# Optimization experiments

Hardware: AMD Instinct MI355X
Metric: run time of the kernel (lower is better)

The kernel has to match this reference:

```python
import jax, jax.numpy as jnp
import numpy as np
from jax import lax

N = 32768      # total nodes (8 graphs x 4096)
E = 262144     # edges (avg degree 8)
B = 8          # graphs in batch
TW = 25        # time window
H = 128        # hidden features
L = 6          # GNN layers
NV = 1         # n_variables (pos_t only)
SD = 1         # spatial dim
TMAX, TMIN, RES_T = 4.0, 0.0, 250.0
BD_LOW, BD_UP = 0.0, 16.0
EPS = 1e-5


def swish(x):
    return x * jax.nn.sigmoid(x)


def setup_inputs() -> dict:
    key = jax.random.key(0)
    ks = jax.random.split(key, 32)
    s = 0.05
    u = jax.random.normal(ks[0], (N, TW), jnp.float32)
    pos_t = jax.random.uniform(ks[1], (N, 1), jnp.float32) * TMAX
    pos_x = jax.random.uniform(ks[2], (N, 1), jnp.float32) * BD_UP
    pos = jnp.concatenate([pos_t, pos_x], axis=-1)
    edge_index = jax.random.randint(ks[3], (2, E), 0, N, jnp.int64)
    batch = jnp.repeat(jnp.arange(B, dtype=jnp.int64), N // B)
    d_in = TW + SD + NV          # 27
    d_msg = 2 * H + TW + SD + NV  # 282
    d_upd = H + H + NV            # 257
    We1 = jax.random.normal(ks[4], (d_in, H), jnp.float32) * s
    be1 = jnp.zeros((H,), jnp.float32)
    We2 = jax.random.normal(ks[5], (H, H), jnp.float32) * s
    be2 = jnp.zeros((H,), jnp.float32)
    Wm1 = jax.random.normal(ks[6], (L, d_msg, H), jnp.float32) * s
    bm1 = jnp.zeros((L, H), jnp.float32)
    Wm2 = jax.random.normal(ks[7], (L, H, H), jnp.float32) * s
    bm2 = jnp.zeros((L, H), jnp.float32)
    Wu1 = jax.random.normal(ks[8], (L, d_upd, H), jnp.float32) * s
    bu1 = jnp.zeros((L, H), jnp.float32)
    Wu2 = jax.random.normal(ks[9], (L, H, H), jnp.float32) * s
    bu2 = jnp.zeros((L, H), jnp.float32)
    Wc1 = jax.random.normal(ks[10], (8, 1, 16), jnp.float32) * s  # OIH
    bc1 = jnp.zeros((8,), jnp.float32)
    Wc2 = jax.random.normal(ks[11], (1, 8, 14), jnp.float32) * s
    bc2 = jnp.zeros((1,), jnp.float32)
    return dict(u=u, pos=pos, edge_index=edge_index, batch=batch,
                We1=We1, be1=be1, We2=We2, be2=be2,
                Wm1=Wm1, bm1=bm1, Wm2=Wm2, bm2=bm2,
                Wu1=Wu1, bu1=bu1, Wu2=Wu2, bu2=bu2,
                Wc1=Wc1, bc1=bc1, Wc2=Wc2, bc2=bc2)


def _mpnn(u, pos, edge_index, batch, We1, be1, We2, be2,
          Wm1, bm1, Wm2, bm2, Wu1, bu1, Wu2, bu2, Wc1, bc1, Wc2, bc2):
    src = edge_index[0]   # j (source)
    tgt = edge_index[1]   # i (target)
    pos_t = pos[:, 0:1] / TMAX
    pos_x = (pos[:, 1:] - BD_LOW) / (BD_UP - BD_LOW)
    variables = pos_t  # eq_variables empty -> only normalized time

    node_input = jnp.concatenate([u, pos_x, variables], axis=-1)  # [N, 27]
    h = swish(node_input @ We1 + be1)
    h = swish(h @ We2 + be2)

    # in-degree for scatter-mean (empty targets -> 0 like PyG mean)
    cnt = jnp.zeros((N,), jnp.float32).at[tgt].add(1.0)
    cnt = jnp.maximum(cnt, 1.0)[:, None]
    # per-graph node counts for InstanceNorm
    gcnt = jax.ops.segment_sum(jnp.ones((N,), jnp.float32), batch, num_segments=B)[:, None]

    u_diff_e = u[tgt] - u[src]          # [E, TW]
    p_diff_e = pos_x[tgt] - pos_x[src]  # [E, SD]
    var_i_e = variables[tgt]            # [E, NV]

    for l in range(L):
        # message: gather -> MLP per edge
        m_in = jnp.concatenate([h[tgt], h[src], u_diff_e, p_diff_e, var_i_e], axis=-1)  # [E, 282]
        msg = swish(m_in @ Wm1[l] + bm1[l])
        msg = swish(msg @ Wm2[l] + bm2[l])
        # scatter-mean aggregate onto targets
        agg = jax.ops.segment_sum(msg, tgt, num_segments=N) / cnt  # [N, H]
        # node update MLP, residual (in_features == out_features)
        up = jnp.concatenate([h, agg, variables], axis=-1)  # [N, 257]
        up = swish(up @ Wu1[l] + bu1[l])
        up = swish(up @ Wu2[l] + bu2[l])
        h = h + up
        # InstanceNorm per graph (no affine), biased variance
        mean = jax.ops.segment_sum(h, batch, num_segments=B) / gcnt      # [B, H]
        sq = jax.ops.segment_sum(h * h, batch, num_segments=B) / gcnt    # [B, H]
        var = sq - mean * mean
        h = (h - mean[batch]) / jnp.sqrt(var[batch] + EPS)

    # output CNN: tw=25 branch
    hc = h[:, None, :]  # [N, 1, 128]
    dn = ('NCH', 'OIH', 'NCH')
    c = lax.conv_general_dilated(hc, Wc1, (3,), 'VALID', dimension_numbers=dn) + bc1[None, :, None]
    c = swish(c)
    c = lax.conv_general_dilated(c, Wc2, (1,), 'VALID', dimension_numbers=dn) + bc2[None, :, None]
    diff = c[:, 0, :]  # [N, 25]

    dt = (TMAX - TMIN) / RES_T
    dt_cum = jnp.arange(1, TW + 1, dtype=jnp.float32) * dt  # cumsum of ones*dt
    out = u[:, -1:] + dt_cum[None, :] * diff
    return out


def reference(u, pos, edge_index, batch, We1, be1, We2, be2,
              Wm1, bm1, Wm2, bm2, Wu1, bu1, Wu2, bu2, Wc1, bc1, Wc2, bc2):
    return _mpnn(u, pos, edge_index, batch, We1, be1, We2, be2,
                 Wm1, bm1, Wm2, bm2, Wu1, bu1, Wu2, bu2, Wc1, bc1, Wc2, bc2)
```

## Files before the change

kernel.cpp:

```cpp
#include <hip/hip_runtime.h>
#include <stdint.h>

#define N_NODES 32768
#define N_EDGES 262144
#define NB 8
#define TW 25

typedef __attribute__((ext_vector_type(8))) short short8;
typedef __attribute__((ext_vector_type(4))) float floatx4;

#if defined(__has_builtin)
#if __has_builtin(__builtin_amdgcn_cvt_pk_bf16_f32)
#define HAVE_CVT_PK_BF16 1
#endif
#endif

__device__ __forceinline__ float swishf(float x) {
    return x * __builtin_amdgcn_rcpf(1.0f + __expf(-x));
}

__device__ __forceinline__ unsigned short f2bf(float x) {
    union { float f; unsigned u; } v; v.f = x;
    unsigned r = v.u + 0x7FFFu + ((v.u >> 16) & 1u);
    return (unsigned short)(r >> 16);
}
__device__ __forceinline__ unsigned pkbf(float a, float b) {
#ifdef HAVE_CVT_PK_BF16
    typedef __attribute__((ext_vector_type(2))) __bf16 bf16x2;
    union { bf16x2 v; unsigned u; } cv;
    cv.v = __builtin_amdgcn_cvt_pk_bf16_f32(a, b);
    return cv.u;
#else
    return (unsigned)f2bf(a) | ((unsigned)f2bf(b) << 16);
#endif
}
__device__ __forceinline__ float bf2f(unsigned short b) {
    union { unsigned u; float f; } v; v.u = ((unsigned)b) << 16; return v.f;
}
__device__ __forceinline__ float bflo(unsigned w) {
    union { unsigned u; float f; } v; v.u = w << 16; return v.f;
}
__device__ __forceinline__ float bfhi(unsigned w) {
    union { unsigned u; float f; } v; v.u = w & 0xffff0000u; return v.f;
}

__global__ void init_kernel(const float* __restrict__ pos, const float* __restrict__ u,
                            float* __restrict__ posx, float* __restrict__ post,
                            unsigned short* __restrict__ feat) {
    int i = blockIdx.x * 256 + threadIdx.x;
    if (i < N_NODES) {
        float pt = pos[i * 2 + 0] * 0.25f;
        float px = pos[i * 2 + 1] * 0.0625f;
        post[i] = pt;
        posx[i] = px;
        unsigned short f[32];
        #pragma unroll
        for (int k = 0; k < 25; ++k) f[k] = f2bf(u[(size_t)i * 25 + k]);
        f[25] = f2bf(px);
        f[26] = f2bf(pt);
        #pragma unroll
        for (int k = 27; k < 32; ++k) f[k] = 0;
        #pragma unroll
        for (int j = 0; j < 4; ++j)
            *(uint4*)(feat + (size_t)i * 32 + j * 8) = *(uint4*)&f[j * 8];
    }
}

__global__ void deg_kernel(const int* __restrict__ tgt, int* __restrict__ deg) {
    int i = blockIdx.x * 256 + threadIdx.x;
    if (i < N_EDGES) atomicAdd(&deg[tgt[i]], 1);
}

__global__ __launch_bounds__(1024) void scan_kernel(const int* __restrict__ deg,
                                                    int* __restrict__ cursor) {
    __shared__ int ps[1024];
    int t = threadIdx.x;
    int base = t * 32;
    int tot = 0;
    for (int i = 0; i < 32; ++i) tot += deg[base + i];
    ps[t] = tot;
    __syncthreads();
    for (int off = 1; off < 1024; off <<= 1) {
        int v = (t >= off) ? ps[t - off] : 0;
        __syncthreads();
        ps[t] += v;
        __syncthreads();
    }
    int run = ps[t] - tot;
    for (int i = 0; i < 32; ++i) {
        cursor[base + i] = run;
        run += deg[base + i];
    }
}

__global__ void scatter_kernel(const int* __restrict__ src, const int* __restrict__ tgt,
                               int* __restrict__ cursor,
                               int* __restrict__ src_s, int* __restrict__ tgt_s) {
    int i = blockIdx.x * 256 + threadIdx.x;
    if (i < N_EDGES) {
        int tg = tgt[i];
        int p = atomicAdd(&cursor[tg], 1);
        src_s[p] = src[i];
        tgt_s[p] = tg;
    }
}

__global__ __launch_bounds__(256) void pack_kernel(const float* __restrict__ W,
                                                   unsigned short* __restrict__ Wp,
                                                   int Kreal, int Kc, int total) {
    int id = blockIdx.x * 256 + threadIdx.x;
    if (id >= total) return;
    int lane = id & 63;
    int t8 = (id >> 6) & 7;
    int rest = id >> 9;
    int c = rest % Kc;
    int l = rest / Kc;
    int n = t8 * 16 + (lane & 15);
    int kb = c * 32 + (lane >> 4) * 8;
    short8 v;
    #pragma unroll
    for (int j = 0; j < 8; ++j) {
        int k = kb + j;
        float x = (k < Kreal) ? W[((size_t)l * Kreal + k) * 128 + n] : 0.f;
        v[j] = (short)f2bf(x);
    }
    *(short8*)(Wp + (size_t)id * 8) = v;
}

__global__ __launch_bounds__(256) void pack_cat_kernel(const float* __restrict__ Wm1,
                                                       unsigned short* __restrict__ Wp) {
    int id = blockIdx.x * 256 + threadIdx.x;
    if (id >= 30720) return;
    int lane = id & 63;
    int tile = (id >> 6) & 15;
    int rest = id >> 10;
    int c = rest % 5;
    int l = rest / 5;
    int n = tile * 16 + (lane & 15);
    int col = n & 127;
    bool isT = n < 128;
    int kb = c * 32 + (lane >> 4) * 8;
    const float* W = Wm1 + (size_t)l * 283 * 128;
    short8 v;
    #pragma unroll
    for (int j = 0; j < 8; ++j) {
        int k = kb + j;
        float x = 0.f;
        if (k < 128) {
            x = W[(size_t)(isT ? k : 128 + k) * 128 + col];
        } else if (k < 155) {
            int row = 256 + (k - 128);
            x = W[(size_t)row * 128 + col];
            if (!isT) x = (row == 282) ? 0.f : -x;
        }
        v[j] = (short)f2bf(x);
    }
    *(short8*)(Wp + (size_t)id * 8) = v;
}

__global__ __launch_bounds__(256) void encoder_kernel(
    const float* __restrict__ u, const float* __restrict__ posx,
    const float* __restrict__ post,
    const float* __restrict__ We1, const float* __restrict__ be1,
    const float* __restrict__ We2, const float* __restrict__ be2,
    unsigned short* __restrict__ hraw, float* __restrict__ agg)
{
    __shared__ __align__(16) float As_[64 * 36];
    __shared__ __align__(16) float Ws[32 * 128];
    __shared__ __align__(16) float Ms[64 * 128];

    int t = threadIdx.x;
    int n0 = blockIdx.x * 64;
    int rg = t >> 5, cg = t & 31;

    {
        int r = t & 63, cseg = t >> 6;
        float4 z = make_float4(0.f, 0.f, 0.f, 0.f);
        #pragma unroll
        for (int j = 0; j < 8; ++j)
            *(float4*)(agg + (size_t)(n0 + r) * 128 + cseg * 32 + j * 4) = z;
    }

    float acc[8][4] = {};
    {
        int kk = t >> 3, cb = (t & 7) * 16;
        #pragma unroll
        for (int j = 0; j < 4; ++j) {
            float4 w = make_float4(0.f, 0.f, 0.f, 0.f);
            if (kk < 27) w = *(const float4*)&We1[kk * 128 + cb + j * 4];
            *(float4*)&Ws[kk * 128 + cb + j * 4] = w;
        }
        int el = t >> 2, kb = (t & 3) * 8, n = n0 + el;
        float v[8];
        #pragma unroll
        for (int j = 0; j < 8; ++j) {
            int k = kb + j;
            float x = 0.f;
            if (k < 25) x = u[n * 25 + k];
            else if (k == 25) x = posx[n];
            else if (k == 26) x = post[n];
            v[j] = x;
        }
        #pragma unroll
        for (int j = 0; j < 8; j += 4)
            *(float4*)&As_[el * 36 + kb + j] = make_float4(v[j], v[j+1], v[j+2], v[j+3]);
        __syncthreads();
        #pragma unroll 4
        for (int kk2 = 0; kk2 < 32; ++kk2) {
            float4 b = *(const float4*)&Ws[kk2 * 128 + cg * 4];
            float a[8];
            #pragma unroll
            for (int i = 0; i < 8; ++i) a[i] = As_[(rg * 8 + i) * 36 + kk2];
            #pragma unroll
            for (int i = 0; i < 8; ++i) {
                acc[i][0] += a[i] * b.x; acc[i][1] += a[i] * b.y;
                acc[i][2] += a[i] * b.z; acc[i][3] += a[i] * b.w;
            }
        }
        __syncthreads();
    }
    {
        float4 b1 = *(const float4*)&be1[cg * 4];
        #pragma unroll
        for (int i = 0; i < 8; ++i) {
            float4 m;
            m.x = swishf(acc[i][0] + b1.x);
            m.y = swishf(acc[i][1] + b1.y);
            m.z = swishf(acc[i][2] + b1.z);
            m.w = swishf(acc[i][3] + b1.w);
            *(float4*)&Ms[(rg * 8 + i) * 128 + cg * 4] = m;
        }
        __syncthreads();
    }
    float acc2[8][4] = {};
    for (int k0 = 0; k0 < 128; k0 += 32) {
        int kk = t >> 3, cb = (t & 7) * 16;
        #pragma unroll
        for (int j = 0; j < 4; ++j)
            *(float4*)&Ws[kk * 128 + cb + j * 4] =
                *(const float4*)&We2[(k0 + kk) * 128 + cb + j * 4];
        __syncthreads();
        #pragma unroll 4
        for (int kk2 = 0; kk2 < 32; ++kk2) {
            float4 b = *(const float4*)&Ws[kk2 * 128 + cg * 4];
            float a[8];
            #pragma unroll
            for (int i = 0; i < 8; ++i) a[i] = Ms[(rg * 8 + i) * 128 + (k0 + kk2)];
            #pragma unroll
            for (int i = 0; i < 8; ++i) {
                acc2[i][0] += a[i] * b.x; acc2[i][1] += a[i] * b.y;
                acc2[i][2] += a[i] * b.z; acc2[i][3] += a[i] * b.w;
            }
        }
        __syncthreads();
    }
    {
        float4 b2 = *(const float4*)&be2[cg * 4];
        #pragma unroll
        for (int i = 0; i < 8; ++i) {
            int n = n0 + rg * 8 + i;
            float4 o;
            o.x = swishf(acc2[i][0] + b2.x);
            o.y = swishf(acc2[i][1] + b2.y);
            o.z = swishf(acc2[i][2] + b2.z);
            o.w = swishf(acc2[i][3] + b2.w);
            uint2 pk;
            pk.x = pkbf(o.x, o.y);
            pk.y = pkbf(o.z, o.w);
            *(uint2*)(hraw + (size_t)n * 128 + cg * 4) = pk;
        }
    }
}

__global__ __launch_bounds__(512, 4) void premsg_kernel(
    const unsigned short* __restrict__ hraw,
    const float* __restrict__ stats, int donorm,
    const unsigned short* __restrict__ feat,
    const unsigned short* __restrict__ Wp, const float* __restrict__ b1,
    unsigned short* __restrict__ h_bf,
    unsigned short* __restrict__ At, unsigned short* __restrict__ As)
{
    __shared__ __align__(16) unsigned short A[64 * 168];
    __shared__ float mean_s[128];
    __shared__ float rstd_s[128];

    int t = threadIdx.x;
    int n0 = blockIdx.x * 64;
    int bidx = n0 >> 12;

    if (t < 128) {
        float mn = 0.f, rs = 1.f;
        if (donorm) {
            float s1 = stats[bidx * 128 + t] * (1.f / 4096.f);
            float s2 = stats[(NB + bidx) * 128 + t] * (1.f / 4096.f);
            mn = s1;
            rs = rsqrtf(s2 - s1 * s1 + 1e-5f);
        }
        mean_s[t] = mn;
        rstd_s[t] = rs;
    }
    __syncthreads();

    {
        int r = t & 63, cseg = t >> 6;
        int n = n0 + r;
        uint4 raw0 = *(const uint4*)(hraw + (size_t)n * 128 + cseg * 16);
        uint4 raw1 = *(const uint4*)(hraw + (size_t)n * 128 + cseg * 16 + 8);
        unsigned pk[8];
        #pragma unroll
        for (int j = 0; j < 8; ++j) {
            unsigned word = (j < 4) ? ((const unsigned*)&raw0)[j]
                                    : ((const unsigned*)&raw1)[j - 4];
            int c0 = cseg * 16 + j * 2;
            float v0 = (bf2f((unsigned short)(word & 0xffffu)) - mean_s[c0]) * rstd_s[c0];
            float v1 = (bf2f((unsigned short)(word >> 16)) - mean_s[c0 + 1]) * rstd_s[c0 + 1];
            pk[j] = pkbf(v0, v1);
        }
        *(uint4*)(A + r * 168 + cseg * 16)     = *(uint4*)&pk[0];
        *(uint4*)(A + r * 168 + cseg * 16 + 8) = *(uint4*)&pk[4];
        *(uint4*)(h_bf + (size_t)n * 128 + cseg * 16)     = *(uint4*)&pk[0];
        *(uint4*)(h_bf + (size_t)n * 128 + cseg * 16 + 8) = *(uint4*)&pk[4];
        if (cseg < 2) {
            uint4 f0 = *(const uint4*)(feat + (size_t)n * 32 + cseg * 16);
            uint4 f1 = *(const uint4*)(feat + (size_t)n * 32 + cseg * 16 + 8);
            *(uint4*)(A + r * 168 + 128 + cseg * 16)     = f0;
            *(uint4*)(A + r * 168 + 128 + cseg * 16 + 8) = f1;
        }
    }
    __syncthreads();

    int w = t >> 6, lane = t & 63, q = lane >> 4, m = lane & 15;
    floatx4 accT[4] = {};
    floatx4 accS[4] = {};
    #pragma unroll
    for (int c = 0; c < 5; ++c) {
        short8 bT = *(const short8*)(Wp + ((size_t)(c * 16 + w) * 64 + lane) * 8);
        short8 bS = *(const short8*)(Wp + ((size_t)(c * 16 + 8 + w) * 64 + lane) * 8);
        #pragma unroll
        for (int g2 = 0; g2 < 4; ++g2) {
            short8 a = *(const short8*)(A + (g2 * 16 + m) * 168 + c * 32 + q * 8);
            accT[g2] = __builtin_amdgcn_mfma_f32_16x16x32_bf16(a, bT, accT[g2], 0, 0, 0);
            accS[g2] = __builtin_amdgcn_mfma_f32_16x16x32_bf16(a, bS, accS[g2], 0, 0, 0);
        }
    }
    int col = w * 16 + m;
    float bv = b1[col];
    #pragma unroll
    for (int g2 = 0; g2 < 4; ++g2) {
        #pragma unroll
        for (int r = 0; r < 4; ++r) {
            int row = g2 * 16 + q * 4 + r;
            At[(size_t)(n0 + row) * 128 + col] = f2bf(accT[g2][r] + bv);
            As[(size_t)(n0 + row) * 128 + col] = f2bf(accS[g2][r]);
        }
    }
}

__global__ __launch_bounds__(256, 8) void message_kernel(
    const unsigned short* __restrict__ At, const unsigned short* __restrict__ As,
    const int* __restrict__ src_s, const int* __restrict__ tgt_s,
    const unsigned short* __restrict__ W2p, const float* __restrict__ b2,
    float* __restrict__ agg, float* __restrict__ stats)
{
    __shared__ __align__(16) unsigned short Cs[64 * 132];
    __shared__ int tgtS[64];

    int t = threadIdx.x;
    int e0 = blockIdx.x * 64;
    if (blockIdx.x == 0) {
        float4 z = make_float4(0.f, 0.f, 0.f, 0.f);
        *(float4*)&stats[t * 8] = z;
        *(float4*)&stats[t * 8 + 4] = z;
    }
    if (t < 64) tgtS[t] = tgt_s[e0 + t];
    __syncthreads();

    int w = t >> 6, lane = t & 63, q = lane >> 4, m = lane & 15;
    int erow = w * 16 + m;
    int e = e0 + erow;
    int gg = tgtS[erow];
    int ss = src_s[e];

    const unsigned short* atp = At + (size_t)gg * 128 + q * 8;
    const unsigned short* asp = As + (size_t)ss * 128 + q * 8;
    uint4 wa[4], wb[4];
    #pragma unroll
    for (int c = 0; c < 4; ++c) {
        wa[c] = *(const uint4*)(atp + c * 32);
        wb[c] = *(const uint4*)(asp + c * 32);
    }
    short8 af[4];
    #pragma unroll
    for (int c = 0; c < 4; ++c) {
        const unsigned* ua = (const unsigned*)&wa[c];
        const unsigned* ub = (const unsigned*)&wb[c];
        union { unsigned u[4]; short8 s; } pk_;
        #pragma unroll
        for (int j = 0; j < 4; ++j) {
            float lo = swishf(bflo(ua[j]) + bflo(ub[j]));
            float hi = swishf(bfhi(ua[j]) + bfhi(ub[j]));
            pk_.u[j] = pkbf(lo, hi);
        }
        af[c] = pk_.s;
    }

    floatx4 acc[8] = {};
    #pragma unroll
    for (int c = 0; c < 4; ++c) {
        #pragma unroll
        for (int t8 = 0; t8 < 8; ++t8) {
            short8 b = *(const short8*)(W2p + ((size_t)(c * 8 + t8) * 64 + lane) * 8);
            acc[t8] = __builtin_amdgcn_mfma_f32_16x16x32_bf16(af[c], b, acc[t8], 0, 0, 0);
        }
    }

    #pragma unroll
    for (int t8 = 0; t8 < 8; ++t8) {
        float bv = b2[t8 * 16 + m];
        unsigned p01 = pkbf(swishf(acc[t8][0] + bv), swishf(acc[t8][1] + bv));
        unsigned p23 = pkbf(swishf(acc[t8][2] + bv), swishf(acc[t8][3] + bv));
        int rb = (w * 16 + q * 4) * 132 + t8 * 16 + m;
        Cs[rb]           = (unsigned short)p01;
        Cs[rb + 132]     = (unsigned short)(p01 >> 16);
        Cs[rb + 2 * 132] = (unsigned short)p23;
        Cs[rb + 3 * 132] = (unsigned short)(p23 >> 16);
    }

    {
        int r0 = w * 16;
        int col0 = lane;
        float run0 = 0.f, run1 = 0.f;
        int prev = tgtS[r0];
        bool atStart = true;
        #pragma unroll 4
        for (int i = 0; i < 16; ++i) {
            int tg = tgtS[r0 + i];
            if (tg != prev) {
                float* d0 = &agg[(size_t)prev * 128 + col0];
                if (atStart) { atomicAdd(d0, run0); atomicAdd(d0 + 64, run1); }
                else         { d0[0] = run0;        d0[64] = run1; }
                run0 = 0.f; run1 = 0.f; prev = tg; atStart = false;
            }
            run0 += bf2f(Cs[(r0 + i) * 132 + col0]);
            run1 += bf2f(Cs[(r0 + i) * 132 + col0 + 64]);
        }
        float* d0 = &agg[(size_t)prev * 128 + col0];
        atomicAdd(d0, run0);
        atomicAdd(d0 + 64, run1);
    }
}

__global__ __launch_bounds__(512, 4) void update_kernel(
    unsigned short* __restrict__ hraw, const unsigned short* __restrict__ h_bf,
    float* __restrict__ agg, const int* __restrict__ deg,
    const float* __restrict__ post,
    const unsigned short* __restrict__ W1p, const float* __restrict__ b1,
    const unsigned short* __restrict__ W2p, const float* __restrict__ b2,
    float* __restrict__ stats)
{
    __shared__ __align__(16) unsigned short SH[64 * 296 + 64 * 136];
    unsigned short* Msh = SH + 64 * 296;

    int t = threadIdx.x;
    int n0 = blockIdx.x * 64;

    {
        int r = t & 63, cseg = t >> 6;
        int n = n0 + r;
        const short8* hn = (const short8*)(h_bf + (size_t)n * 128);
        #pragma unroll
        for (int j = 0; j < 2; ++j) {
            int chunk = cseg * 2 + j;
            *(short8*)(SH + r * 296 + chunk * 8) = hn[chunk];
        }
        float ic = __builtin_amdgcn_rcpf(fmaxf((float)deg[n], 1.0f));
        #pragma unroll
        for (int j = 0; j < 2; ++j) {
            int unit = cseg * 2 + j;
            const float* ap = agg + (size_t)n * 128 + unit * 8;
            float4 v0 = *(const float4*)ap;
            float4 v1 = *(const float4*)(ap + 4);
            unsigned pa[4];
            pa[0] = pkbf(v0.x * ic, v0.y * ic);
            pa[1] = pkbf(v0.z * ic, v0.w * ic);
            pa[2] = pkbf(v1.x * ic, v1.y * ic);
            pa[3] = pkbf(v1.z * ic, v1.w * ic);
            *(uint4*)(SH + r * 296 + 128 + unit * 8) = *(uint4*)pa;
        }
        if (cseg < 4) {
            short8 z;
            #pragma unroll
            for (int k = 0; k < 8; ++k) z[k] = 0;
            if (cseg == 0) z[0] = (short)f2bf(post[n]);
            *(short8*)(SH + r * 296 + 256 + cseg * 8) = z;
        }
    }
    __syncthreads();

    int w = t >> 6, lane = t & 63, q = lane >> 4, m = lane & 15;

    floatx4 acc[4] = {};
    #pragma unroll
    for (int c = 0; c < 9; ++c) {
        short8 b = *(const short8*)(W1p + ((size_t)(c * 8 + w) * 64 + lane) * 8);
        #pragma unroll
        for (int g2 = 0; g2 < 4; ++g2) {
            short8 a = *(const short8*)(SH + (g2 * 16 + m) * 296 + c * 32 + q * 8);
            acc[g2] = __builtin_amdgcn_mfma_f32_16x16x32_bf16(a, b, acc[g2], 0, 0, 0);
        }
    }
    {
        int col = w * 16 + m;
        float bv = b1[col];
        #pragma unroll
        for (int g2 = 0; g2 < 4; ++g2) {
            unsigned p01 = pkbf(swishf(acc[g2][0] + bv), swishf(acc[g2][1] + bv));
            unsigned p23 = pkbf(swishf(acc[g2][2] + bv), swishf(acc[g2][3] + bv));
            int base = g2 * 16 + q * 4;
            Msh[(base + 0) * 136 + col] = (unsigned short)p01;
            Msh[(base + 1) * 136 + col] = (unsigned short)(p01 >> 16);
            Msh[(base + 2) * 136 + col] = (unsigned short)p23;
            Msh[(base + 3) * 136 + col] = (unsigned short)(p23 >> 16);
        }
    }
    __syncthreads();

    floatx4 acc2[4] = {};
    #pragma unroll
    for (int c = 0; c < 4; ++c) {
        short8 b = *(const short8*)(W2p + ((size_t)(c * 8 + w) * 64 + lane) * 8);
        #pragma unroll
        for (int g2 = 0; g2 < 4; ++g2) {
            short8 a = *(const short8*)(Msh + (g2 * 16 + m) * 136 + c * 32 + q * 8);
            acc2[g2] = __builtin_amdgcn_mfma_f32_16x16x32_bf16(a, b, acc2[g2], 0, 0, 0);
        }
    }

    int bidx = n0 >> 12;
    int col = w * 16 + m;
    float bv = b2[col];
    float s = 0.f, s2 = 0.f;
    #pragma unroll
    for (int g2 = 0; g2 < 4; ++g2) {
        #pragma unroll
        for (int r = 0; r < 4; ++r) {
            int row = g2 * 16 + q * 4 + r;
            float res = bf2f(SH[row * 296 + col]);
            float hv = res + swishf(acc2[g2][r] + bv);
            hraw[(size_t)(n0 + row) * 128 + col] = f2bf(hv);
            s += hv; s2 += hv * hv;
        }
    }
    s  += __shfl_xor(s, 16);  s  += __shfl_xor(s, 32);
    s2 += __shfl_xor(s2, 16); s2 += __shfl_xor(s2, 32);
    if (q == 0) {
        atomicAdd(&stats[bidx * 128 + col], s);
        atomicAdd(&stats[(NB + bidx) * 128 + col], s2);
    }
    {
        int r = t & 63, cseg = t >> 6;
        float4 z = make_float4(0.f, 0.f, 0.f, 0.f);
        #pragma unroll
        for (int j = 0; j < 4; ++j)
            *(float4*)(agg + (size_t)(n0 + r) * 128 + cseg * 16 + j * 4) = z;
    }
}

__global__ __launch_bounds__(256) void conv_kernel(
    const unsigned short* __restrict__ hraw, const float* __restrict__ stats,
    const float* __restrict__ u,
    const float* __restrict__ Wc1, const float* __restrict__ bc1,
    const float* __restrict__ Wc2, const float* __restrict__ bc2,
    float* __restrict__ out)
{
    __shared__ float hs[4][128];
    __shared__ float c1[4][8 * 40];
    int w = threadIdx.x >> 6, lane = threadIdx.x & 63;
    int n = blockIdx.x * 4 + w;
    int b = n >> 12;
    #pragma unroll
    for (int h2 = 0; h2 < 2; ++h2) {
        int c = lane + h2 * 64;
        float s1 = stats[b * 128 + c] * (1.f / 4096.f);
        float s2 = stats[(NB + b) * 128 + c] * (1.f / 4096.f);
        float rs = rsqrtf(s2 - s1 * s1 + 1e-5f);
        hs[w][c] = (bf2f(hraw[(size_t)n * 128 + c]) - s1) * rs;
    }
    __syncthreads();
    for (int idx = lane; idx < 304; idx += 64) {
        int o = idx / 38, p = idx % 38;
        float s = bc1[o];
        #pragma unroll
        for (int k = 0; k < 16; ++k) s += hs[w][p * 3 + k] * Wc1[o * 16 + k];
        c1[w][o * 40 + p] = swishf(s);
    }
    __syncthreads();
    if (lane < TW) {
        float s = bc2[0];
        #pragma unroll
        for (int o = 0; o < 8; ++o)
            for (int k = 0; k < 14; ++k)
                s += c1[w][o * 40 + lane + k] * Wc2[o * 14 + k];
        float dt_cum = (float)(lane + 1) * (4.0f / 250.0f);
        out[n * TW + lane] = u[n * 25 + 24] + dt_cum * s;
    }
}

extern "C" void kernel_launch(void* const* d_in, const int* in_sizes, int n_in,
                              void* d_out, int out_size, void* d_ws, size_t ws_size,
                              hipStream_t stream)
{
    const float* u   = (const float*)d_in[0];
    const float* pos = (const float*)d_in[1];
    const int*   ei  = (const int*)d_in[2];
    const float* We1 = (const float*)d_in[4];
    const float* be1 = (const float*)d_in[5];
    const float* We2 = (const float*)d_in[6];
    const float* be2 = (const float*)d_in[7];
    const float* Wm1 = (const float*)d_in[8];
    const float* bm1 = (const float*)d_in[9];
    const float* Wm2 = (const float*)d_in[10];
    const float* bm2 = (const float*)d_in[11];
    const float* Wu1 = (const float*)d_in[12];
    const float* bu1 = (const float*)d_in[13];
    const float* Wu2 = (const float*)d_in[14];
    const float* bu2 = (const float*)d_in[15];
    const float* Wc1 = (const float*)d_in[16];
    const float* bc1 = (const float*)d_in[17];
    const float* Wc2 = (const float*)d_in[18];
    const float* bc2 = (const float*)d_in[19];
    float* out = (float*)d_out;

    char* base = (char*)d_ws;
    size_t off = 0;
    auto alloc = [&](size_t bytes) -> char* {
        char* r = base + off;
        off = (off + bytes + 511) & ~(size_t)511;
        return r;
    };
    unsigned short* hraw   = (unsigned short*)alloc((size_t)N_NODES * 128 * 2);
    unsigned short* h_bf   = (unsigned short*)alloc((size_t)N_NODES * 128 * 2);
    float*          agg    = (float*)alloc((size_t)N_NODES * 128 * 4);
    unsigned short* At     = (unsigned short*)alloc((size_t)N_NODES * 128 * 2);
    unsigned short* As     = (unsigned short*)alloc((size_t)N_NODES * 128 * 2);
    float*          posx   = (float*)alloc(N_NODES * 4);
    float*          post   = (float*)alloc(N_NODES * 4);
    unsigned short* feat   = (unsigned short*)alloc((size_t)N_NODES * 32 * 2);
    float*          stats  = (float*)alloc(2 * NB * 128 * 4);
    int*            deg    = (int*)alloc(N_NODES * 4);
    int*            cursor = (int*)alloc(N_NODES * 4);
    int*            src_s  = (int*)alloc((size_t)N_EDGES * 4);
    int*            tgt_s  = (int*)alloc((size_t)N_EDGES * 4);
    unsigned short* Wcat1p = (unsigned short*)alloc((size_t)6 * 5 * 16 * 64 * 8 * 2);
    unsigned short* Wm2p   = (unsigned short*)alloc((size_t)6 * 4 * 4096 * 2);
    unsigned short* Wu1p   = (unsigned short*)alloc((size_t)6 * 9 * 4096 * 2);
    unsigned short* Wu2p   = (unsigned short*)alloc((size_t)6 * 4 * 4096 * 2);
    (void)ws_size;

    const int* srcp = ei;
    const int* tgtp = ei + N_EDGES;

    init_kernel<<<N_NODES / 256, 256, 0, stream>>>(pos, u, posx, post, feat);
    hipMemsetAsync(deg, 0, N_NODES * sizeof(int), stream);
    deg_kernel<<<N_EDGES / 256, 256, 0, stream>>>(tgtp, deg);
    scan_kernel<<<1, 1024, 0, stream>>>(deg, cursor);
    scatter_kernel<<<N_EDGES / 256, 256, 0, stream>>>(srcp, tgtp, cursor, src_s, tgt_s);
    encoder_kernel<<<N_NODES / 64, 256, 0, stream>>>(u, posx, post, We1, be1, We2, be2,
                                                     hraw, agg);
    {
        pack_cat_kernel<<<120, 256, 0, stream>>>(Wm1, Wcat1p);
        int tot1 = 6 * 9 * 512;
        int tot2 = 6 * 4 * 512;
        pack_kernel<<<(tot2 + 255) / 256, 256, 0, stream>>>(Wm2, Wm2p, 128, 4, tot2);
        pack_kernel<<<(tot1 + 255) / 256, 256, 0, stream>>>(Wu1, Wu1p, 257, 9, tot1);
        pack_kernel<<<(tot2 + 255) / 256, 256, 0, stream>>>(Wu2, Wu2p, 128, 4, tot2);
    }

    for (int l = 0; l < 6; ++l) {
        premsg_kernel<<<N_NODES / 64, 512, 0, stream>>>(
            hraw, stats, (l > 0) ? 1 : 0, feat,
            Wcat1p + (size_t)l * 5 * 16 * 64 * 8, bm1 + l * 128,
            h_bf, At, As);
        message_kernel<<<N_EDGES / 64, 256, 0, stream>>>(
            At, As, src_s, tgt_s,
            Wm2p + (size_t)l * 4 * 4096, bm2 + l * 128, agg, stats);
        update_kernel<<<N_NODES / 64, 512, 0, stream>>>(
            hraw, h_bf, agg, deg, post,
            Wu1p + (size_t)l * 9 * 4096, bu1 + l * 128,
            Wu2p + (size_t)l * 4 * 4096, bu2 + l * 128, stats);
    }

    conv_kernel<<<N_NODES / 4, 256, 0, stream>>>(hraw, stats, u, Wc1, bc1, Wc2, bc2, out);
}
```

Before: 637.6 us.

## Fuse update-MLP h-projection into premsg GEMM and shrink update kernel K

The h-dependent part of the first update-MLP layer (h·Wu1[:128] + bias) is now computed in premsg alongside the message T/S projections, using a third MFMA accumulator, and stored as a bf16 Uh buffer. The update kernel then only multiplies the [agg, pos_t] slice (K=160 instead of 288), using smaller shared memory and higher occupancy. In the message kernel, target indices are loaded directly without a block barrier, and a sched_barrier plus a changed occupancy bound are added. The trade-off is an extra bf16 write and read of Uh per layer, plus rounding of the partial sum to bf16.

After: 628.6 us. Within noise of the previous version (-1.4%).

```diff
diff --git a/kernel.cpp b/kernel.cpp
--- a/kernel.cpp
+++ b/kernel.cpp
@@ -128,31 +128,60 @@
 }
 
 __global__ __launch_bounds__(256) void pack_cat_kernel(const float* __restrict__ Wm1,
+                                                       const float* __restrict__ Wu1,
                                                        unsigned short* __restrict__ Wp) {
     int id = blockIdx.x * 256 + threadIdx.x;
-    if (id >= 30720) return;
+    if (id >= 46080) return;
     int lane = id & 63;
-    int tile = (id >> 6) & 15;
-    int rest = id >> 10;
-    int c = rest % 5;
-    int l = rest / 5;
+    int tmp = id >> 6;
+    int tile = tmp % 24;
+    int tmp2 = tmp / 24;
+    int c = tmp2 % 5;
+    int l = tmp2 / 5;
     int n = tile * 16 + (lane & 15);
+    int grp = n >> 7;
     int col = n & 127;
-    bool isT = n < 128;
     int kb = c * 32 + (lane >> 4) * 8;
-    const float* W = Wm1 + (size_t)l * 283 * 128;
+    const float* Wm = Wm1 + (size_t)l * 283 * 128;
+    const float* Wu = Wu1 + (size_t)l * 257 * 128;
     short8 v;
     #pragma unroll
     for (int j = 0; j < 8; ++j) {
         int k = kb + j;
         float x = 0.f;
-        if (k < 128) {
-            x = W[(size_t)(isT ? k : 128 + k) * 128 + col];
+        if (grp == 2) {
+            if (k < 128) x = Wu[(size_t)k * 128 + col];
+        } else if (k < 128) {
+            x = Wm[(size_t)(grp ? 128 + k : k) * 128 + col];
         } else if (k < 155) {
             int row = 256 + (k - 128);
-            x = W[(size_t)row * 128 + col];
-            if (!isT) x = (row == 282) ? 0.f : -x;
-        }
+            x = Wm[(size_t)row * 128 + col];
+            if (grp) x = (row == 282) ? 0.f : -x;
+        }
+        v[j] = (short)f2bf(x);
+    }
+    *(short8*)(Wp + (size_t)id * 8) = v;
+}
+
+__global__ __launch_bounds__(256) void pack_upd_kernel(const float* __restrict__ Wu1,
+                                                       unsigned short* __restrict__ Wp) {
+    int id = blockIdx.x * 256 + threadIdx.x;
+    if (id >= 15360) return;
+    int lane = id & 63;
+    int t8 = (id >> 6) & 7;
+    int rest = id >> 9;
+    int c = rest % 5;
+    int l = rest / 5;
+    int n = t8 * 16 + (lane & 15);
+    int kb = c * 32 + (lane >> 4) * 8;
+    const float* Wu = Wu1 + (size_t)l * 257 * 128;
+    short8 v;
+    #pragma unroll
+    for (int j = 0; j < 8; ++j) {
+        int k = kb + j;
+        float x = 0.f;
+        if (k < 128) x = Wu[(size_t)(128 + k) * 128 + n];
+        else if (k == 128) x = Wu[(size_t)256 * 128 + n];
         v[j] = (short)f2bf(x);
     }
     *(short8*)(Wp + (size_t)id * 8) = v;
@@ -276,9 +305,11 @@
     const unsigned short* __restrict__ hraw,
     const float* __restrict__ stats, int donorm,
     const unsigned short* __restrict__ feat,
-    const unsigned short* __restrict__ Wp, const float* __restrict__ b1,
+    const unsigned short* __restrict__ Wp,
+    const float* __restrict__ b1, const float* __restrict__ bu1,
     unsigned short* __restrict__ h_bf,
-    unsigned short* __restrict__ At, unsigned short* __restrict__ As)
+    unsigned short* __restrict__ At, unsigned short* __restrict__ As,
+    unsigned short* __restrict__ Uh)
 {
     __shared__ __align__(16) unsigned short A[64 * 168];
     __shared__ float mean_s[128];
@@ -332,31 +363,37 @@
     int w = t >> 6, lane = t & 63, q = lane >> 4, m = lane & 15;
     floatx4 accT[4] = {};
     floatx4 accS[4] = {};
+    floatx4 accU[4] = {};
     #pragma unroll
     for (int c = 0; c < 5; ++c) {
-        short8 bT = *(const short8*)(Wp + ((size_t)(c * 16 + w) * 64 + lane) * 8);
-        short8 bS = *(const short8*)(Wp + ((size_t)(c * 16 + 8 + w) * 64 + lane) * 8);
+        short8 bT = *(const short8*)(Wp + ((size_t)(c * 24 + w) * 64 + lane) * 8);
+        short8 bS = *(const short8*)(Wp + ((size_t)(c * 24 + 8 + w) * 64 + lane) * 8);
+        short8 bU = *(const short8*)(Wp + ((size_t)(c * 24 + 16 + w) * 64 + lane) * 8);
         #pragma unroll
         for (int g2 = 0; g2 < 4; ++g2) {
             short8 a = *(const short8*)(A + (g2 * 16 + m) * 168 + c * 32 + q * 8);
             accT[g2] = __builtin_amdgcn_mfma_f32_16x16x32_bf16(a, bT, accT[g2], 0, 0, 0);
             accS[g2] = __builtin_amdgcn_mfma_f32_16x16x32_bf16(a, bS, accS[g2], 0, 0, 0);
+            accU[g2] = __builtin_amdgcn_mfma_f32_16x16x32_bf16(a, bU, accU[g2], 0, 0, 0);
         }
     }
     int col = w * 16 + m;
-    float bv = b1[col];
+    float bvT = b1[col];
+    float bvU = bu1[col];
     #pragma unroll
     for (int g2 = 0; g2 < 4; ++g2) {
         #pragma unroll
         for (int r = 0; r < 4; ++r) {
             int row = g2 * 16 + q * 4 + r;
-            At[(size_t)(n0 + row) * 128 + col] = f2bf(accT[g2][r] + bv);
-            As[(size_t)(n0 + row) * 128 + col] = f2bf(accS[g2][r]);
-        }
-    }
-}
-
-__global__ __launch_bounds__(256, 8) void message_kernel(
+            size_t idx = (size_t)(n0 + row) * 128 + col;
+            At[idx] = f2bf(accT[g2][r] + bvT);
+            As[idx] = f2bf(accS[g2][r]);
+            Uh[idx] = f2bf(accU[g2][r] + bvU);
+        }
+    }
+}
+
+__global__ __launch_bounds__(256, 6) void message_kernel(
     const unsigned short* __restrict__ At, const unsigned short* __restrict__ As,
     const int* __restrict__ src_s, const int* __restrict__ tgt_s,
     const unsigned short* __restrict__ W2p, const float* __restrict__ b2,
@@ -372,14 +409,13 @@
         *(float4*)&stats[t * 8] = z;
         *(float4*)&stats[t * 8 + 4] = z;
     }
-    if (t < 64) tgtS[t] = tgt_s[e0 + t];
-    __syncthreads();
 
     int w = t >> 6, lane = t & 63, q = lane >> 4, m = lane & 15;
     int erow = w * 16 + m;
     int e = e0 + erow;
-    int gg = tgtS[erow];
+    int gg = tgt_s[e];
     int ss = src_s[e];
+    if (lane < 16) tgtS[w * 16 + lane] = tgt_s[e0 + w * 16 + lane];
 
     const unsigned short* atp = At + (size_t)gg * 128 + q * 8;
     const unsigned short* asp = As + (size_t)ss * 128 + q * 8;
@@ -389,6 +425,8 @@
         wa[c] = *(const uint4*)(atp + c * 32);
         wb[c] = *(const uint4*)(asp + c * 32);
     }
+    __builtin_amdgcn_sched_barrier(0);
+
     short8 af[4];
     #pragma unroll
     for (int c = 0; c < 4; ++c) {
@@ -450,16 +488,17 @@
     }
 }
 
-__global__ __launch_bounds__(512, 4) void update_kernel(
+__global__ __launch_bounds__(512, 8) void update_kernel(
     unsigned short* __restrict__ hraw, const unsigned short* __restrict__ h_bf,
+    const unsigned short* __restrict__ Uh,
     float* __restrict__ agg, const int* __restrict__ deg,
     const float* __restrict__ post,
-    const unsigned short* __restrict__ W1p, const float* __restrict__ b1,
+    const unsigned short* __restrict__ W1p,
     const unsigned short* __restrict__ W2p, const float* __restrict__ b2,
     float* __restrict__ stats)
 {
-    __shared__ __align__(16) unsigned short SH[64 * 296 + 64 * 136];
-    unsigned short* Msh = SH + 64 * 296;
+    __shared__ __align__(16) unsigned short A[64 * 168];
+    __shared__ __align__(16) unsigned short Msh[64 * 136];
 
     int t = threadIdx.x;
     int n0 = blockIdx.x * 64;
@@ -467,60 +506,60 @@
     {
         int r = t & 63, cseg = t >> 6;
         int n = n0 + r;
-        const short8* hn = (const short8*)(h_bf + (size_t)n * 128);
-        #pragma unroll
-        for (int j = 0; j < 2; ++j) {
-            int chunk = cseg * 2 + j;
-            *(short8*)(SH + r * 296 + chunk * 8) = hn[chunk];
-        }
         float ic = __builtin_amdgcn_rcpf(fmaxf((float)deg[n], 1.0f));
-        #pragma unroll
-        for (int j = 0; j < 2; ++j) {
-            int unit = cseg * 2 + j;
-            const float* ap = agg + (size_t)n * 128 + unit * 8;
-            float4 v0 = *(const float4*)ap;
-            float4 v1 = *(const float4*)(ap + 4);
-            unsigned pa[4];
-            pa[0] = pkbf(v0.x * ic, v0.y * ic);
-            pa[1] = pkbf(v0.z * ic, v0.w * ic);
-            pa[2] = pkbf(v1.x * ic, v1.y * ic);
-            pa[3] = pkbf(v1.z * ic, v1.w * ic);
-            *(uint4*)(SH + r * 296 + 128 + unit * 8) = *(uint4*)pa;
-        }
+        const float* ap = agg + (size_t)n * 128 + cseg * 16;
+        float4 v0 = *(const float4*)ap;
+        float4 v1 = *(const float4*)(ap + 4);
+        float4 v2 = *(const float4*)(ap + 8);
+        float4 v3 = *(const float4*)(ap + 12);
+        unsigned pa[8];
+        pa[0] = pkbf(v0.x * ic, v0.y * ic);
+        pa[1] = pkbf(v0.z * ic, v0.w * ic);
+        pa[2] = pkbf(v1.x * ic, v1.y * ic);
+        pa[3] = pkbf(v1.z * ic, v1.w * ic);
+        pa[4] = pkbf(v2.x * ic, v2.y * ic);
+        pa[5] = pkbf(v2.z * ic, v2.w * ic);
+        pa[6] = pkbf(v3.x * ic, v3.y * ic);
+        pa[7] = pkbf(v3.z * ic, v3.w * ic);
+        *(uint4*)(A + r * 168 + cseg * 16)     = *(uint4*)&pa[0];
+        *(uint4*)(A + r * 168 + cseg * 16 + 8) = *(uint4*)&pa[4];
         if (cseg < 4) {
             short8 z;
             #pragma unroll
             for (int k = 0; k < 8; ++k) z[k] = 0;
             if (cseg == 0) z[0] = (short)f2bf(post[n]);
-            *(short8*)(SH + r * 296 + 256 + cseg * 8) = z;
+            *(short8*)(A + r * 168 + 128 + cseg * 8) = z;
         }
     }
     __syncthreads();
 
     int w = t >> 6, lane = t & 63, q = lane >> 4, m = lane & 15;
+    int col = w * 16 + m;
 
     floatx4 acc[4] = {};
     #pragma unroll
-    for (int c = 0; c < 9; ++c) {
+    for (int c = 0; c < 5; ++c) {
         short8 b = *(const short8*)(W1p + ((size_t)(c * 8 + w) * 64 + lane) * 8);
         #pragma unroll
         for (int g2 = 0; g2 < 4; ++g2) {
-            short8 a = *(const short8*)(SH + (g2 * 16 + m) * 296 + c * 32 + q * 8);
+            short8 a = *(const short8*)(A + (g2 * 16 + m) * 168 + c * 32 + q * 8);
             acc[g2] = __builtin_amdgcn_mfma_f32_16x16x32_bf16(a, b, acc[g2], 0, 0, 0);
         }
     }
     {
-        int col = w * 16 + m;
-        float bv = b1[col];
         #pragma unroll
         for (int g2 = 0; g2 < 4; ++g2) {
-            unsigned p01 = pkbf(swishf(acc[g2][0] + bv), swishf(acc[g2][1] + bv));
-            unsigned p23 = pkbf(swishf(acc[g2][2] + bv), swishf(acc[g2][3] + bv));
-            int base = g2 * 16 + q * 4;
-            Msh[(base + 0) * 136 + col] = (unsigned short)p01;
-            Msh[(base + 1) * 136 + col] = (unsigned short)(p01 >> 16);
-            Msh[(base + 2) * 136 + col] = (unsigned short)p23;
-            Msh[(base + 3) * 136 + col] = (unsigned short)(p23 >> 16);
+            int rowb = g2 * 16 + q * 4;
+            float v0 = swishf(acc[g2][0] + bf2f(Uh[(size_t)(n0 + rowb + 0) * 128 + col]));
+            float v1 = swishf(acc[g2][1] + bf2f(Uh[(size_t)(n0 + rowb + 1) * 128 + col]));
+            float v2 = swishf(acc[g2][2] + bf2f(Uh[(size_t)(n0 + rowb + 2) * 128 + col]));
+            float v3 = swishf(acc[g2][3] + bf2f(Uh[(size_t)(n0 + rowb + 3) * 128 + col]));
+            unsigned p01 = pkbf(v0, v1);
+            unsigned p23 = pkbf(v2, v3);
+            Msh[(rowb + 0) * 136 + col] = (unsigned short)p01;
+            Msh[(rowb + 1) * 136 + col] = (unsigned short)(p01 >> 16);
+            Msh[(rowb + 2) * 136 + col] = (unsigned short)p23;
+            Msh[(rowb + 3) * 136 + col] = (unsigned short)(p23 >> 16);
         }
     }
     __syncthreads();
@@ -537,7 +576,6 @@
     }
 
     int bidx = n0 >> 12;
-    int col = w * 16 + m;
     float bv = b2[col];
     float s = 0.f, s2 = 0.f;
     #pragma unroll
@@ -545,7 +583,7 @@
         #pragma unroll
         for (int r = 0; r < 4; ++r) {
             int row = g2 * 16 + q * 4 + r;
-            float res = bf2f(SH[row * 296 + col]);
+            float res = bf2f(h_bf[(size_t)(n0 + row) * 128 + col]);
             float hv = res + swishf(acc2[g2][r] + bv);
             hraw[(size_t)(n0 + row) * 128 + col] = f2bf(hv);
             s += hv; s2 += hv * hv;
@@ -643,6 +681,7 @@
     float*          agg    = (float*)alloc((size_t)N_NODES * 128 * 4);
     unsigned short* At     = (unsigned short*)alloc((size_t)N_NODES * 128 * 2);
     unsigned short* As     = (unsigned short*)alloc((size_t)N_NODES * 128 * 2);
+    unsigned short* Uh     = (unsigned short*)alloc((size_t)N_NODES * 128 * 2);
     float*          posx   = (float*)alloc(N_NODES * 4);
     float*          post   = (float*)alloc(N_NODES * 4);
     unsigned short* feat   = (unsigned short*)alloc((size_t)N_NODES * 32 * 2);
@@ -651,9 +690,9 @@
     int*            cursor = (int*)alloc(N_NODES * 4);
     int*            src_s  = (int*)alloc((size_t)N_EDGES * 4);
     int*            tgt_s  = (int*)alloc((size_t)N_EDGES * 4);
-    unsigned short* Wcat1p = (unsigned short*)alloc((size_t)6 * 5 * 16 * 64 * 8 * 2);
+    unsigned short* Wcat1p = (unsigned short*)alloc((size_t)46080 * 8 * 2);
     unsigned short* Wm2p   = (unsigned short*)alloc((size_t)6 * 4 * 4096 * 2);
-    unsigned short* Wu1p   = (unsigned short*)alloc((size_t)6 * 9 * 4096 * 2);
+    unsigned short* Wu1p   = (unsigned short*)alloc((size_t)15360 * 8 * 2);
     unsigned short* Wu2p   = (unsigned short*)alloc((size_t)6 * 4 * 4096 * 2);
     (void)ws_size;
 
@@ -668,25 +707,24 @@
     encoder_kernel<<<N_NODES / 64, 256, 0, stream>>>(u, posx, post, We1, be1, We2, be2,
                                                      hraw, agg);
     {
-        pack_cat_kernel<<<120, 256, 0, stream>>>(Wm1, Wcat1p);
-        int tot1 = 6 * 9 * 512;
+        pack_cat_kernel<<<180, 256, 0, stream>>>(Wm1, Wu1, Wcat1p);
+        pack_upd_kernel<<<60, 256, 0, stream>>>(Wu1, Wu1p);
         int tot2 = 6 * 4 * 512;
         pack_kernel<<<(tot2 + 255) / 256, 256, 0, stream>>>(Wm2, Wm2p, 128, 4, tot2);
-        pack_kernel<<<(tot1 + 255) / 256, 256, 0, stream>>>(Wu1, Wu1p, 257, 9, tot1);
         pack_kernel<<<(tot2 + 255) / 256, 256, 0, stream>>>(Wu2, Wu2p, 128, 4, tot2);
     }
 
     for (int l = 0; l < 6; ++l) {
         premsg_kernel<<<N_NODES / 64, 512, 0, stream>>>(
             hraw, stats, (l > 0) ? 1 : 0, feat,
-            Wcat1p + (size_t)l * 5 * 16 * 64 * 8, bm1 + l * 128,
-            h_bf, At, As);
+            Wcat1p + (size_t)l * 5 * 24 * 512, bm1 + l * 128, bu1 + l * 128,
+            h_bf, At, As, Uh);
         message_kernel<<<N_EDGES / 64, 256, 0, stream>>>(
             At, As, src_s, tgt_s,
             Wm2p + (size_t)l * 4 * 4096, bm2 + l * 128, agg, stats);
         update_kernel<<<N_NODES / 64, 512, 0, stream>>>(
-            hraw, h_bf, agg, deg, post,
-            Wu1p + (size_t)l * 9 * 4096, bu1 + l * 128,
+            hraw, h_bf, Uh, agg, deg, post,
+            Wu1p + (size_t)l * 5 * 8 * 512,
             Wu2p + (size_t)l * 4 * 4096, bu2 + l * 128, stats);
     }
 
```
